# Optimization experiments

Hardware: AMD Instinct MI355X
Metric: run time of the kernel (lower is better)

Reference implementation:

```python
import jax, jax.numpy as jnp
import numpy as np

EMBED = 768
HEADS = 12
FACTOR = 2
LN_EPS = 1e-5


def layer_norm(x, gamma, beta):
    mu = jnp.mean(x, axis=-1, keepdims=True)
    var = jnp.mean(jnp.square(x - mu), axis=-1, keepdims=True)
    return (x - mu) * jax.lax.rsqrt(var + LN_EPS) * gamma + beta


def setup_inputs() -> dict:
    key = jax.random.key(0)
    ks = jax.random.split(key, 8)
    B, S, E = 8, 1024, EMBED
    H = FACTOR * E
    s_e = 1.0 / np.sqrt(E)
    s_h = 1.0 / np.sqrt(H)
    return {
        "x": jax.random.normal(ks[0], (B, S, E), jnp.float32),
        "Wq": jax.random.normal(ks[1], (E, E), jnp.float32) * s_e,
        "Wk": jax.random.normal(ks[2], (E, E), jnp.float32) * s_e,
        "Wv": jax.random.normal(ks[3], (E, E), jnp.float32) * s_e,
        "W1": jax.random.normal(ks[4], (E, H), jnp.float32) * s_e,
        "b1": jnp.zeros((H,), jnp.float32),
        "W2": jax.random.normal(ks[5], (H, E), jnp.float32) * s_h,
        "b2": jnp.zeros((E,), jnp.float32),
        "g1": jnp.ones((E,), jnp.float32),
        "beta1": jnp.zeros((E,), jnp.float32),
        "g2": jnp.ones((E,), jnp.float32),
        "beta2": jnp.zeros((E,), jnp.float32),
    }


def reference(x, Wq, Wk, Wv, W1, b1, W2, b2, g1, beta1, g2, beta2):
    B, S, E = x.shape
    hd = E // HEADS
    # NOTE: original reshapes (B,S,E)->(B,H,S,hd) WITHOUT transposing heads
    # (non-standard: mixes sequence blocks across heads) - replicated faithfully.
    q = (x @ Wq).reshape(B, HEADS, S, hd)
    k = (x @ Wk).reshape(B, HEADS, S, hd)
    v = (x @ Wv).reshape(B, HEADS, S, hd)
    # no 1/sqrt(d) scaling in the original
    attn = jax.nn.softmax(jnp.einsum('bnqd,bnkd->bnqk', q, k), axis=-1)
    # NOTE: original einsum 'bnqk,bnvd->bnqd' sums over BOTH k and v
    # (value is sum-pooled over its sequence axis) - replicated faithfully.
    out = jnp.einsum('bnqk,bnvd->bnqd', attn, v)
    out = out.transpose(0, 2, 1, 3).reshape(B, S, E)
    a = x + layer_norm(out, g1, beta1)
    # GELU after BOTH linears (exact GELU, torch default)
    h = jax.nn.gelu(a @ W1 + b1, approximate=False)
    m = jax.nn.gelu(h @ W2 + b2, approximate=False)
    return x + layer_norm(m, g2, beta2)
```

## Files before the change

### kernel.cpp

```cpp
#include <hip/hip_runtime.h>
#include <hip/hip_bf16.h>
#include <math.h>

#define E_ 768
#define HID_ 1536
#define SQ_ 1024

typedef unsigned short u16;
using bf16x8 = __attribute__((ext_vector_type(8))) __bf16;
using f32x4  = __attribute__((ext_vector_type(4))) float;

__device__ __forceinline__ u16 f2bf(float f) {
  union { float f; unsigned u; } v; v.f = f;
  unsigned r = v.u + 0x7FFFu + ((v.u >> 16) & 1u);
  return (u16)(r >> 16);
}
__device__ __forceinline__ float bf2f(u16 h) {
  union { unsigned u; float f; } v; v.u = ((unsigned)h) << 16; return v.f;
}
__device__ __forceinline__ float gelu_f(float x) {
  return 0.5f * x * (1.0f + erff(x * 0.70710678118654752f));
}

#define GLDS16(gp, sp) __builtin_amdgcn_global_load_lds( \
    (__attribute__((address_space(1))) const void*)(const void*)(gp), \
    (__attribute__((address_space(3))) void*)(void*)(sp), 16, 0, 0)

__global__ void prep_kernel(const float* __restrict__ x, const float* __restrict__ W1,
                            const float* __restrict__ W2, u16* __restrict__ xb,
                            u16* __restrict__ W1T, u16* __restrict__ W2T) {
  __shared__ float T[64 * 65];
  int bid = blockIdx.x, t = threadIdx.x;
  if (bid < 6144) {
    int base = bid * 1024 + t * 4;
    const float4 v = *reinterpret_cast<const float4*>(x + base);
    ushort4 o; o.x = f2bf(v.x); o.y = f2bf(v.y); o.z = f2bf(v.z); o.w = f2bf(v.w);
    *reinterpret_cast<ushort4*>(xb + base) = o;
    return;
  }
  const float* in; u16* out; int R_in, C_in, rt, ct;
  if (bid < 6432) {
    int b2 = bid - 6144; in = W1; out = W1T; R_in = 768; C_in = 1536;
    rt = b2 / 24; ct = b2 % 24;
  } else {
    int b3 = bid - 6432; in = W2; out = W2T; R_in = 1536; C_in = 768;
    rt = b3 / 12; ct = b3 % 12;
  }
  int r0 = rt << 6, c0 = ct << 6;
  int tr = t >> 4, tc4 = (t & 15) << 2;
#pragma unroll
  for (int i = 0; i < 4; ++i) {
    int row = tr + (i << 4);
    const float4 v = *reinterpret_cast<const float4*>(in + (size_t)(r0 + row) * C_in + c0 + tc4);
    T[row * 65 + tc4 + 0] = v.x;
    T[row * 65 + tc4 + 1] = v.y;
    T[row * 65 + tc4 + 2] = v.z;
    T[row * 65 + tc4 + 3] = v.w;
  }
  __syncthreads();
#pragma unroll
  for (int i = 0; i < 4; ++i) {
    int orow = tr + (i << 4);
    ushort4 o;
    o.x = f2bf(T[(tc4 + 0) * 65 + orow]);
    o.y = f2bf(T[(tc4 + 1) * 65 + orow]);
    o.z = f2bf(T[(tc4 + 2) * 65 + orow]);
    o.w = f2bf(T[(tc4 + 3) * 65 + orow]);
    *reinterpret_cast<ushort4*>(out + (size_t)(c0 + orow) * R_in + r0 + tc4) = o;
  }
}

__global__ void ypath_kernel(const u16* __restrict__ xb, const float* __restrict__ Wv,
                             float* __restrict__ Y) {
  int r = blockIdx.x;
  int b = r / 12, n = r % 12;
  int t = threadIdx.x;
  int u0 = n << 10;
  int s_lo = u0 / 12;
  int s_hi = (u0 + 1023) / 12;
  float acc[12][3];
#pragma unroll
  for (int g = 0; g < 12; ++g)
    for (int q = 0; q < 3; ++q) acc[g][q] = 0.f;
  const u16* xp = xb + (size_t)b * SQ_ * E_;
  for (int s = s_lo; s <= s_hi; ++s) {
    float v0 = bf2f(xp[(size_t)s * E_ + t]);
    float v1 = bf2f(xp[(size_t)s * E_ + t + 256]);
    float v2 = bf2f(xp[(size_t)s * E_ + t + 512]);
    int du = 12 * s - u0;
    if (du >= 0 && du <= 1012) {
#pragma unroll
      for (int g = 0; g < 12; ++g) { acc[g][0] += v0; acc[g][1] += v1; acc[g][2] += v2; }
    } else {
#pragma unroll
      for (int g = 0; g < 12; ++g) {
        int u = du + g;
        if (u >= 0 && u < 1024) { acc[g][0] += v0; acc[g][1] += v1; acc[g][2] += v2; }
      }
    }
  }
  __shared__ float Ls[12 * 768];
#pragma unroll
  for (int g = 0; g < 12; ++g) {
    Ls[g * 768 + t]       = acc[g][0];
    Ls[g * 768 + t + 256] = acc[g][1];
    Ls[g * 768 + t + 512] = acc[g][2];
  }
  __syncthreads();
  int d = t & 63, sub = t >> 6;
  float part[12];
#pragma unroll
  for (int g = 0; g < 12; ++g) part[g] = 0.f;
  int j0 = sub * 192;
  for (int jj = 0; jj < 192; ++jj) {
    int j = j0 + jj;
    const float* wp = Wv + (size_t)j * 768 + d;
#pragma unroll
    for (int g = 0; g < 12; ++g)
      part[g] += Ls[g * 768 + j] * wp[g * 64];
  }
  __shared__ float red[4][12][64];
#pragma unroll
  for (int g = 0; g < 12; ++g) red[sub][g][d] = part[g];
  __syncthreads();
  if (t < 64) {
    float s = 0.f;
#pragma unroll
    for (int su = 0; su < 4; ++su)
#pragma unroll
      for (int g = 0; g < 12; ++g) s += red[su][g][t];
    Y[r * 64 + t] = s;
  }
}

__global__ void c1_kernel(const float* __restrict__ Y, const float* __restrict__ g1,
                          const float* __restrict__ be1, const float* __restrict__ W1,
                          const float* __restrict__ b1, float* __restrict__ C1) {
  int bid = blockIdx.x;
  int b = bid / 48, c = bid % 48;
  int t = threadIdx.x;
  __shared__ float Ls[768];
  __shared__ float red[8][32];
  __shared__ float red2[8];
  float y0 = Y[b * 768 + t];
  float y1 = Y[b * 768 + t + 256];
  float y2 = Y[b * 768 + t + 512];
  float s = y0 + y1 + y2;
  float sq = y0 * y0 + y1 * y1 + y2 * y2;
#pragma unroll
  for (int o = 32; o > 0; o >>= 1) { s += __shfl_down(s, o, 64); sq += __shfl_down(sq, o, 64); }
  if ((t & 63) == 0) { red2[(t >> 6) * 2] = s; red2[(t >> 6) * 2 + 1] = sq; }
  __syncthreads();
  s  = red2[0] + red2[2] + red2[4] + red2[6];
  sq = red2[1] + red2[3] + red2[5] + red2[7];
  float mu = s * (1.f / 768.f);
  float var = sq * (1.f / 768.f) - mu * mu;
  float rsv = rsqrtf(var + 1e-5f);
  Ls[t]       = (y0 - mu) * rsv * g1[t]       + be1[t];
  Ls[t + 256] = (y1 - mu) * rsv * g1[t + 256] + be1[t + 256];
  Ls[t + 512] = (y2 - mu) * rsv * g1[t + 512] + be1[t + 512];
  __syncthreads();
  int tc = t & 31, ts = t >> 5;
  int n = c * 32 + tc;
  float acc = 0.f;
  int j0 = ts * 96;
#pragma unroll 4
  for (int j = j0; j < j0 + 96; ++j) acc += Ls[j] * W1[(size_t)j * HID_ + n];
  red[ts][tc] = acc;
  __syncthreads();
  if (ts == 0) {
    float sv = b1[n];
#pragma unroll
    for (int k = 0; k < 8; ++k) sv += red[k][tc];
    C1[b * HID_ + n] = sv;
  }
}

template <int MODE>
__global__ __launch_bounds__(256, 2) void gemm_bt_kernel(
    const u16* __restrict__ A, const u16* __restrict__ BT,
    const float* __restrict__ bias, void* __restrict__ out0, void* __restrict__ out1,
    int N, int lda, int ldb) {
  __shared__ __align__(16) u16 As[128 * 64];
  __shared__ __align__(16) u16 Bs[128 * 64];
  int bid = blockIdx.x;
  int xcd = bid & 7, idx = bid >> 3;
  int mloc, n_, k_off, kk = 0;
  if (MODE == 0) { mloc = idx / 12; n_ = idx % 12; k_off = 0; }
  else           { kk = idx / 48; int rem = idx % 48; mloc = rem / 6; n_ = rem % 6; k_off = kk * 768; }
  int bm = (xcd * 8 + mloc) << 7, bn = n_ << 7;

  int t = threadIdx.x;
  int lane = t & 63, w = t >> 6;
  int wm = (w >> 1) << 6, wn = (w & 1) << 6;
  int quad = lane >> 4, l16 = lane & 15;
  f32x4 acc[4][4] = {};

  for (int k0 = 0; k0 < 768; k0 += 64) {
    __syncthreads();
#pragma unroll
    for (int i = 0; i < 4; ++i) {
      int ci = t + (i << 8);
      int r = ci >> 3, csw = ci & 7;
      int kc = csw ^ (r & 7);
      const u16* ga = A + (size_t)(bm + r) * lda + k_off + k0 + (kc << 3);
      GLDS16(ga, As + ci * 8);
      const u16* gb = BT + (size_t)(bn + r) * ldb + k_off + k0 + (kc << 3);
      GLDS16(gb, Bs + ci * 8);
    }
    __builtin_amdgcn_s_waitcnt(0);
    __syncthreads();
#pragma unroll
    for (int ks = 0; ks < 2; ++ks) {
      bf16x8 af[4], bf[4];
      int kc = (ks << 2) + quad;
#pragma unroll
      for (int mt = 0; mt < 4; ++mt) {
        int row = wm + (mt << 4) + l16;
        af[mt] = *reinterpret_cast<const bf16x8*>(As + row * 64 + ((kc ^ (row & 7)) << 3));
      }
#pragma unroll
      for (int nt = 0; nt < 4; ++nt) {
        int row = wn + (nt << 4) + l16;
        bf[nt] = *reinterpret_cast<const bf16x8*>(Bs + row * 64 + ((kc ^ (row & 7)) << 3));
      }
#pragma unroll
      for (int mt = 0; mt < 4; ++mt)
#pragma unroll
        for (int nt = 0; nt < 4; ++nt)
          acc[mt][nt] = __builtin_amdgcn_mfma_f32_16x16x32_bf16(af[mt], bf[nt], acc[mt][nt], 0, 0, 0);
    }
  }

#pragma unroll
  for (int mt = 0; mt < 4; ++mt) {
    int row0 = bm + wm + (mt << 4) + (quad << 2);
#pragma unroll
    for (int nt = 0; nt < 4; ++nt) {
      int col = bn + wn + (nt << 4) + l16;
      float bv = (MODE == 0) ? bias[(bm >> 10) * N + col] : 0.f;
#pragma unroll
      for (int rr = 0; rr < 4; ++rr) {
        float v = acc[mt][nt][rr] + bv;
        size_t idxo = (size_t)(row0 + rr) * N + col;
        if (MODE == 0)       ((u16*)out0)[idxo] = f2bf(gelu_f(v));
        else if (kk == 0)    ((u16*)out0)[idxo] = f2bf(v);
        else                 ((u16*)out1)[idxo] = f2bf(v);
      }
    }
  }
}

__global__ void ln2_kernel(const u16* __restrict__ p0, const u16* __restrict__ p1,
                           const float* __restrict__ x, const float* __restrict__ b2,
                           const float* __restrict__ g2, const float* __restrict__ be2,
                           float* __restrict__ out) {
  int row = blockIdx.x, t = threadIdx.x;
  float v0 = 0.f, v1 = 0.f, v2 = 0.f, v3 = 0.f;
  float s = 0.f, sq = 0.f;
  int e = t << 2;
  if (t < 192) {
    ushort4 pa = *reinterpret_cast<const ushort4*>(p0 + (size_t)row * 768 + e);
    ushort4 pb = *reinterpret_cast<const ushort4*>(p1 + (size_t)row * 768 + e);
    float4 bb = *reinterpret_cast<const float4*>(b2 + e);
    v0 = gelu_f(bf2f(pa.x) + bf2f(pb.x) + bb.x);
    v1 = gelu_f(bf2f(pa.y) + bf2f(pb.y) + bb.y);
    v2 = gelu_f(bf2f(pa.z) + bf2f(pb.z) + bb.z);
    v3 = gelu_f(bf2f(pa.w) + bf2f(pb.w) + bb.w);
    s = (v0 + v1) + (v2 + v3);
    sq = (v0 * v0 + v1 * v1) + (v2 * v2 + v3 * v3);
  }
  __shared__ float red[8];
#pragma unroll
  for (int o = 32; o > 0; o >>= 1) { s += __shfl_down(s, o, 64); sq += __shfl_down(sq, o, 64); }
  if ((t & 63) == 0) { red[(t >> 6) * 2] = s; red[(t >> 6) * 2 + 1] = sq; }
  __syncthreads();
  s  = red[0] + red[2] + red[4];
  sq = red[1] + red[3] + red[5];
  float mu = s * (1.f / 768.f);
  float var = sq * (1.f / 768.f) - mu * mu;
  float rs = rsqrtf(var + 1e-5f);
  if (t < 192) {
    float4 gg = *reinterpret_cast<const float4*>(g2 + e);
    float4 be = *reinterpret_cast<const float4*>(be2 + e);
    float4 xx = *reinterpret_cast<const float4*>(x + (size_t)row * 768 + e);
    float4 o;
    o.x = xx.x + (v0 - mu) * rs * gg.x + be.x;
    o.y = xx.y + (v1 - mu) * rs * gg.y + be.y;
    o.z = xx.z + (v2 - mu) * rs * gg.z + be.z;
    o.w = xx.w + (v3 - mu) * rs * gg.w + be.w;
    *reinterpret_cast<float4*>(out + (size_t)row * 768 + e) = o;
  }
}

extern "C" void kernel_launch(void* const* d_in, const int* in_sizes, int n_in,
                              void* d_out, int out_size, void* d_ws, size_t ws_size,
                              hipStream_t stream) {
  const float* x   = (const float*)d_in[0];
  const float* Wv  = (const float*)d_in[3];
  const float* W1  = (const float*)d_in[4];
  const float* b1  = (const float*)d_in[5];
  const float* W2  = (const float*)d_in[6];
  const float* b2  = (const float*)d_in[7];
  const float* g1  = (const float*)d_in[8];
  const float* be1 = (const float*)d_in[9];
  const float* g2  = (const float*)d_in[10];
  const float* be2 = (const float*)d_in[11];
  float* out = (float*)d_out;

  char* ws = (char*)d_ws;
  u16*   xb  = (u16*)(ws);
  u16*   W1T = (u16*)(ws + 12582912);
  u16*   W2T = (u16*)(ws + 14942208);
  u16*   h   = (u16*)(ws + 17301504);
  float* Y   = (float*)(ws + 42467328);
  float* C1  = (float*)(ws + 42491904);
  u16*   m0  = (u16*)(ws + 42541056);
  u16*   p1  = xb;

  prep_kernel<<<6720, 256, 0, stream>>>(x, W1, W2, xb, W1T, W2T);
  ypath_kernel<<<96, 256, 0, stream>>>(xb, Wv, Y);
  c1_kernel<<<384, 256, 0, stream>>>(Y, g1, be1, W1, b1, C1);
  gemm_bt_kernel<0><<<768, 256, 0, stream>>>(xb, W1T, C1, (void*)h, nullptr, 1536, 768, 768);
  gemm_bt_kernel<1><<<768, 256, 0, stream>>>(h, W2T, nullptr, (void*)m0, (void*)p1, 768, 1536, 1536);
  ln2_kernel<<<8192, 256, 0, stream>>>(m0, p1, x, b2, g2, be2, out);
}
```

Baseline: 249.0 us.

## Split value-path reduction into parallel rowsum and Wv-projection kernels with atomics

The single 96-block ypath kernel is split in two. A 384-block rowsum kernel writes per-chunk partial sums to workspace (aliased over the h buffer). A 384-block yfin kernel reduces those partials, multiplies a quarter of Wv and atomically adds into Y, which is zeroed by the first kernel. This exposes more parallelism on a serial stage that only used 96 blocks, at the cost of an extra launch, workspace traffic and float atomics that make the summation order nondeterministic. ln2 also now launches 192 threads per row instead of 256 and drops the idle-thread guards.

New measurement: 219.0 us. 1.14x faster.

```diff
diff --git a/kernel.cpp b/kernel.cpp
--- a/kernel.cpp
+++ b/kernel.cpp
@@ -70,56 +70,84 @@
   }
 }
 
-__global__ void ypath_kernel(const u16* __restrict__ xb, const float* __restrict__ Wv,
-                             float* __restrict__ Y) {
-  int r = blockIdx.x;
+__global__ void rowsum_kernel(const u16* __restrict__ xb, float* __restrict__ Rp,
+                              float* __restrict__ Y) {
+  int bid = blockIdx.x;
+  int r = bid >> 2, c = bid & 3;
   int b = r / 12, n = r % 12;
   int t = threadIdx.x;
+  if (bid == 0) {
+#pragma unroll
+    for (int i = 0; i < 24; ++i) Y[t + i * 256] = 0.f;
+  }
   int u0 = n << 10;
   int s_lo = u0 / 12;
   int s_hi = (u0 + 1023) / 12;
+  int cnt = s_hi - s_lo + 1;
+  int cs = s_lo + (cnt * c) / 4;
+  int ce = s_lo + (cnt * (c + 1)) / 4;
   float acc[12][3];
 #pragma unroll
   for (int g = 0; g < 12; ++g)
     for (int q = 0; q < 3; ++q) acc[g][q] = 0.f;
   const u16* xp = xb + (size_t)b * SQ_ * E_;
-  for (int s = s_lo; s <= s_hi; ++s) {
+  for (int s = cs; s < ce; ++s) {
     float v0 = bf2f(xp[(size_t)s * E_ + t]);
     float v1 = bf2f(xp[(size_t)s * E_ + t + 256]);
     float v2 = bf2f(xp[(size_t)s * E_ + t + 512]);
     int du = 12 * s - u0;
-    if (du >= 0 && du <= 1012) {
-#pragma unroll
-      for (int g = 0; g < 12; ++g) { acc[g][0] += v0; acc[g][1] += v1; acc[g][2] += v2; }
-    } else {
-#pragma unroll
-      for (int g = 0; g < 12; ++g) {
-        int u = du + g;
-        if (u >= 0 && u < 1024) { acc[g][0] += v0; acc[g][1] += v1; acc[g][2] += v2; }
-      }
+#pragma unroll
+    for (int g = 0; g < 12; ++g) {
+      int u = du + g;
+      if (u >= 0 && u < 1024) { acc[g][0] += v0; acc[g][1] += v1; acc[g][2] += v2; }
     }
   }
-  __shared__ float Ls[12 * 768];
+  float* Rr = Rp + (size_t)bid * 9216;
 #pragma unroll
   for (int g = 0; g < 12; ++g) {
-    Ls[g * 768 + t]       = acc[g][0];
-    Ls[g * 768 + t + 256] = acc[g][1];
-    Ls[g * 768 + t + 512] = acc[g][2];
+    Rr[g * 768 + t]       = acc[g][0];
+    Rr[g * 768 + t + 256] = acc[g][1];
+    Rr[g * 768 + t + 512] = acc[g][2];
+  }
+}
+
+__global__ __launch_bounds__(256, 4) void yfin_kernel(
+    const float* __restrict__ Rp, const float* __restrict__ Wv,
+    float* __restrict__ Y) {
+  int bid = blockIdx.x;
+  int r = bid >> 2, jq = bid & 3;
+  int t = threadIdx.x;
+  __shared__ float Ls[12 * 192];
+  __shared__ float red[4][12][64];
+  const float* Rb = Rp + (size_t)r * 4 * 9216 + jq * 192;
+  for (int i = t; i < 576; i += 256) {
+    int g = i / 48, off = (i % 48) << 2;
+    const float* p = Rb + g * 768 + off;
+    float4 v0 = *reinterpret_cast<const float4*>(p);
+    float4 v1 = *reinterpret_cast<const float4*>(p + 9216);
+    float4 v2 = *reinterpret_cast<const float4*>(p + 18432);
+    float4 v3 = *reinterpret_cast<const float4*>(p + 27648);
+    float4 s4;
+    s4.x = (v0.x + v1.x) + (v2.x + v3.x);
+    s4.y = (v0.y + v1.y) + (v2.y + v3.y);
+    s4.z = (v0.z + v1.z) + (v2.z + v3.z);
+    s4.w = (v0.w + v1.w) + (v2.w + v3.w);
+    *reinterpret_cast<float4*>(&Ls[g * 192 + off]) = s4;
   }
   __syncthreads();
   int d = t & 63, sub = t >> 6;
   float part[12];
 #pragma unroll
   for (int g = 0; g < 12; ++g) part[g] = 0.f;
-  int j0 = sub * 192;
-  for (int jj = 0; jj < 192; ++jj) {
-    int j = j0 + jj;
-    const float* wp = Wv + (size_t)j * 768 + d;
+  int jl0 = sub * 48;
+  const float* wp = Wv + (size_t)(jq * 192) * 768 + d;
+  for (int jj = 0; jj < 48; ++jj) {
+    int jl = jl0 + jj;
+    const float* wj = wp + (size_t)jl * 768;
 #pragma unroll
     for (int g = 0; g < 12; ++g)
-      part[g] += Ls[g * 768 + j] * wp[g * 64];
-  }
-  __shared__ float red[4][12][64];
+      part[g] += Ls[g * 192 + jl] * wj[g * 64];
+  }
 #pragma unroll
   for (int g = 0; g < 12; ++g) red[sub][g][d] = part[g];
   __syncthreads();
@@ -129,7 +157,7 @@
     for (int su = 0; su < 4; ++su)
 #pragma unroll
       for (int g = 0; g < 12; ++g) s += red[su][g][t];
-    Y[r * 64 + t] = s;
+    atomicAdd(&Y[r * 64 + t], s);
   }
 }
 
@@ -256,20 +284,16 @@
                            const float* __restrict__ g2, const float* __restrict__ be2,
                            float* __restrict__ out) {
   int row = blockIdx.x, t = threadIdx.x;
-  float v0 = 0.f, v1 = 0.f, v2 = 0.f, v3 = 0.f;
-  float s = 0.f, sq = 0.f;
   int e = t << 2;
-  if (t < 192) {
-    ushort4 pa = *reinterpret_cast<const ushort4*>(p0 + (size_t)row * 768 + e);
-    ushort4 pb = *reinterpret_cast<const ushort4*>(p1 + (size_t)row * 768 + e);
-    float4 bb = *reinterpret_cast<const float4*>(b2 + e);
-    v0 = gelu_f(bf2f(pa.x) + bf2f(pb.x) + bb.x);
-    v1 = gelu_f(bf2f(pa.y) + bf2f(pb.y) + bb.y);
-    v2 = gelu_f(bf2f(pa.z) + bf2f(pb.z) + bb.z);
-    v3 = gelu_f(bf2f(pa.w) + bf2f(pb.w) + bb.w);
-    s = (v0 + v1) + (v2 + v3);
-    sq = (v0 * v0 + v1 * v1) + (v2 * v2 + v3 * v3);
-  }
+  ushort4 pa = *reinterpret_cast<const ushort4*>(p0 + (size_t)row * 768 + e);
+  ushort4 pb = *reinterpret_cast<const ushort4*>(p1 + (size_t)row * 768 + e);
+  float4 bb = *reinterpret_cast<const float4*>(b2 + e);
+  float v0 = gelu_f(bf2f(pa.x) + bf2f(pb.x) + bb.x);
+  float v1 = gelu_f(bf2f(pa.y) + bf2f(pb.y) + bb.y);
+  float v2 = gelu_f(bf2f(pa.z) + bf2f(pb.z) + bb.z);
+  float v3 = gelu_f(bf2f(pa.w) + bf2f(pb.w) + bb.w);
+  float s = (v0 + v1) + (v2 + v3);
+  float sq = (v0 * v0 + v1 * v1) + (v2 * v2 + v3 * v3);
   __shared__ float red[8];
 #pragma unroll
   for (int o = 32; o > 0; o >>= 1) { s += __shfl_down(s, o, 64); sq += __shfl_down(sq, o, 64); }
@@ -280,17 +304,15 @@
   float mu = s * (1.f / 768.f);
   float var = sq * (1.f / 768.f) - mu * mu;
   float rs = rsqrtf(var + 1e-5f);
-  if (t < 192) {
-    float4 gg = *reinterpret_cast<const float4*>(g2 + e);
-    float4 be = *reinterpret_cast<const float4*>(be2 + e);
-    float4 xx = *reinterpret_cast<const float4*>(x + (size_t)row * 768 + e);
-    float4 o;
-    o.x = xx.x + (v0 - mu) * rs * gg.x + be.x;
-    o.y = xx.y + (v1 - mu) * rs * gg.y + be.y;
-    o.z = xx.z + (v2 - mu) * rs * gg.z + be.z;
-    o.w = xx.w + (v3 - mu) * rs * gg.w + be.w;
-    *reinterpret_cast<float4*>(out + (size_t)row * 768 + e) = o;
-  }
+  float4 gg = *reinterpret_cast<const float4*>(g2 + e);
+  float4 be = *reinterpret_cast<const float4*>(be2 + e);
+  float4 xx = *reinterpret_cast<const float4*>(x + (size_t)row * 768 + e);
+  float4 o;
+  o.x = xx.x + (v0 - mu) * rs * gg.x + be.x;
+  o.y = xx.y + (v1 - mu) * rs * gg.y + be.y;
+  o.z = xx.z + (v2 - mu) * rs * gg.z + be.z;
+  o.w = xx.w + (v3 - mu) * rs * gg.w + be.w;
+  *reinterpret_cast<float4*>(out + (size_t)row * 768 + e) = o;
 }
 
 extern "C" void kernel_launch(void* const* d_in, const int* in_sizes, int n_in,
@@ -313,15 +335,17 @@
   u16*   W1T = (u16*)(ws + 12582912);
   u16*   W2T = (u16*)(ws + 14942208);
   u16*   h   = (u16*)(ws + 17301504);
-  float* Y   = (float*)(ws + 42467328);
-  float* C1  = (float*)(ws + 42491904);
-  u16*   m0  = (u16*)(ws + 42541056);
+  float* Rp  = (float*)(ws + 17301504);
+  float* Y   = (float*)(ws + 44826624);
+  float* C1  = (float*)(ws + 44875776);
+  u16*   m0  = (u16*)(ws + 44924928);
   u16*   p1  = xb;
 
   prep_kernel<<<6720, 256, 0, stream>>>(x, W1, W2, xb, W1T, W2T);
-  ypath_kernel<<<96, 256, 0, stream>>>(xb, Wv, Y);
+  rowsum_kernel<<<384, 256, 0, stream>>>(xb, Rp, Y);
+  yfin_kernel<<<384, 256, 0, stream>>>(Rp, Wv, Y);
   c1_kernel<<<384, 256, 0, stream>>>(Y, g1, be1, W1, b1, C1);
   gemm_bt_kernel<0><<<768, 256, 0, stream>>>(xb, W1T, C1, (void*)h, nullptr, 1536, 768, 768);
   gemm_bt_kernel<1><<<768, 256, 0, stream>>>(h, W2T, nullptr, (void*)m0, (void*)p1, 768, 1536, 1536);
-  ln2_kernel<<<8192, 256, 0, stream>>>(m0, p1, x, b2, g2, be2, out);
-}
+  ln2_kernel<<<8192, 192, 0, stream>>>(m0, p1, x, b2, g2, be2, out);
+}
```
